# Kernel tuning notes

Hardware: AMD Instinct MI355X
Metric: run time of the kernel (lower is better)

The kernel has to match this reference:

```python
import jax, jax.numpy as jnp
import numpy as np

N_ATOMS = 30000
N_PAIRS = 1200000
N_BASIS = 7
N_RADIAL = 5
N_SPECIES = 119
R_MIN = 0.5
R_MAX = 6.0
UNITS = (512, 512)
BOX = 6.0  # Angstrom box edge so many pairs fall inside the cutoff
N_FEAT = 360  # gaussian-moment feature count for n_radial=5

# static triangular index sets (fully symmetric contractions)
_TRI2_I, _TRI2_J = np.triu_indices(N_RADIAL)
_TRI3 = np.array([(i, j, k) for i in range(N_RADIAL)
                  for j in range(i, N_RADIAL)
                  for k in range(j, N_RADIAL)], dtype=np.int32)


def setup_inputs() -> dict:
    key = jax.random.key(0)
    ks = jax.random.split(key, 8)
    R = jax.random.uniform(ks[0], (N_ATOMS, 3), jnp.float32) * BOX
    Z = jax.random.randint(ks[1], (N_ATOMS,), 0, N_SPECIES, dtype=jnp.int32)
    idx = jax.random.randint(ks[2], (2, N_PAIRS), 0, N_ATOMS, dtype=jnp.int32)
    W_radial = jax.random.normal(ks[3], (N_SPECIES, N_SPECIES, N_RADIAL, N_BASIS), jnp.float32) / np.sqrt(N_BASIS)
    w1 = jax.random.normal(ks[4], (N_FEAT, UNITS[0]), jnp.float32) / np.sqrt(N_FEAT)
    b1 = jnp.zeros((UNITS[0],), jnp.float32)
    w2 = jax.random.normal(ks[5], (UNITS[0], UNITS[1]), jnp.float32) / np.sqrt(UNITS[0])
    b2 = jnp.zeros((UNITS[1],), jnp.float32)
    w3 = jax.random.normal(ks[6], (UNITS[1], 1), jnp.float32) / np.sqrt(UNITS[1])
    b3 = jnp.zeros((1,), jnp.float32)
    scale = 2.0 * jnp.ones((N_SPECIES, 1), jnp.float32)
    shift = 1.0 * jnp.ones((N_SPECIES, 1), jnp.float32)
    return dict(R=R, Z=Z, idx=idx, W_radial=W_radial, w1=w1, b1=b1,
                w2=w2, b2=b2, w3=w3, b3=b3, scale=scale, shift=shift)


def _descriptor(R, Z, idx, W_radial):
    idx_i, idx_j = idx[0], idx[1]
    # pairwise displacement (free-space displacement fn)
    dr_vec = R[idx_j] - R[idx_i]                                  # [P,3]
    dr = jnp.sqrt(jnp.sum(dr_vec * dr_vec, axis=-1) + 1e-12)      # [P]
    dn = dr_vec / (dr + 1e-5)[:, None]                            # unit vectors [P,3]

    # gaussian radial basis
    betta = N_BASIS ** 2 / R_MAX ** 2
    rad_norm = (2.0 * betta / np.pi) ** 0.25
    shifts = R_MIN + (R_MAX - R_MIN) / N_BASIS * jnp.arange(N_BASIS, dtype=jnp.float32)
    basis = rad_norm * jnp.exp(-betta * (dr[:, None] - shifts) ** 2)  # [P,B]

    # cosine cutoff and per species-pair embedding of the basis
    cutoff = 0.5 * (jnp.cos(jnp.pi * dr / R_MAX) + 1.0) * (dr < R_MAX)
    coeffs = W_radial[Z[idx_i], Z[idx_j]]                          # [P,K,B] irregular gather
    radial = jnp.einsum('pkb,pb->pk', coeffs, basis)               # [P,K]
    radial = radial * (cutoff / np.sqrt(N_BASIS))[:, None]

    seg = lambda x: jax.ops.segment_sum(x, idx_i, num_segments=N_ATOMS)
    # geometric moments of order 0..3
    m0 = seg(radial)                                               # [A,K]
    m1 = seg(radial[:, :, None] * dn[:, None, :])                  # [A,K,3]
    dn2 = dn[:, :, None] * dn[:, None, :]                          # [P,3,3]
    m2 = seg(radial[:, :, None, None] * dn2[:, None])              # [A,K,3,3]
    dn3 = dn2[:, :, :, None] * dn[:, None, None, :]                # [P,3,3,3]
    m3 = seg(radial[:, :, None, None, None] * dn3[:, None])        # [A,K,3,3,3]

    # gaussian-moment invariant contractions
    c1 = jnp.einsum('ari,asi->ars', m1, m1)
    c2 = jnp.einsum('arij,asij->ars', m2, m2)
    c3 = jnp.einsum('arijk,asijk->ars', m3, m3)
    c4 = jnp.einsum('arij,asik,atjk->arst', m2, m2, m2)
    c5 = jnp.einsum('ari,asj,atij->arst', m1, m1, m2)
    c6 = jnp.einsum('arijk,asijl,atkl->arst', m3, m3, m2)
    c7 = jnp.einsum('arijk,asij,atk->arst', m3, m2, m1)

    A = m0.shape[0]
    gm = jnp.concatenate([
        m0,
        c1[:, _TRI2_I, _TRI2_J],
        c2[:, _TRI2_I, _TRI2_J],
        c3[:, _TRI2_I, _TRI2_J],
        c4[:, _TRI3[:, 0], _TRI3[:, 1], _TRI3[:, 2]],
        c5[:, _TRI2_I, _TRI2_J, :].reshape(A, -1),
        c6[:, _TRI2_I, _TRI2_J, :].reshape(A, -1),
        c7.reshape(A, -1),
    ], axis=-1)                                                    # [A,360]
    return gm


def reference(R, Z, idx, W_radial, w1, b1, w2, b2, w3, b3, scale, shift):
    gm = _descriptor(R, Z, idx, W_radial)
    h = jax.nn.swish(gm @ w1 + b1)
    h = jax.nn.swish(h @ w2 + b2)
    h = h @ w3 + b3                                                # [A,1]
    return scale[Z] * h + shift[Z]
```

## Files before the change

### kernel.cpp

```cpp
#include <hip/hip_runtime.h>

#define NA      30000
#define MPAD    30080
#define NPAIRS  1200000
#define NB      7
#define NK      5
#define NSP     119
#define NFEAT   360
#define KP1     384
#define NU      512
#define WROWH   40
#define MAXSLOT 120
#define PSTRIDE 128
#define NBK     118
#define BCAP    11520
#define PPB     4688
#define NTILE   235

#define BETTA      1.3611111111111112f
#define RADNORM    0.96481348f
#define SHIFT_STEP 0.7857142857142857f
#define PI_OVER_R  0.5235987755982988f
#define INV_SQRT7  0.3779644730092272f
#define RMAXV      6.0f
#define TCOEF      2.138888888888889f

typedef __attribute__((ext_vector_type(8))) short bf16x8;
typedef __attribute__((ext_vector_type(4))) float f32x4;
typedef __attribute__((ext_vector_type(2))) float f32x2;
typedef __attribute__((ext_vector_type(4))) unsigned int u32x4;
typedef _Float16 h16x2 __attribute__((ext_vector_type(2)));

__device__ __forceinline__ unsigned short f2b(float x) {
    unsigned u = __float_as_uint(x);
    unsigned r = u + 0x7FFF + ((u >> 16) & 1);
    return (unsigned short)(r >> 16);
}

__global__ __launch_bounds__(256)
void k_part(const int* __restrict__ idx, const int* __restrict__ Z,
            int* __restrict__ gcur, int* __restrict__ part) {
    __shared__ int hist[NBK];
    __shared__ int base[NBK];
    int tid = threadIdx.x;
    for (int b = tid; b < NBK; b += 256) hist[b] = 0;
    __syncthreads();
    int p0 = blockIdx.x * PPB;
    int p1 = min(p0 + PPB, NPAIRS);
    for (int p = p0 + tid; p < p1; p += 256)
        atomicAdd(&hist[idx[p] >> 8], 1);
    __syncthreads();
    for (int b = tid; b < NBK; b += 256) {
        base[b] = atomicAdd(&gcur[b], hist[b]);
        hist[b] = 0;
    }
    __syncthreads();
    for (int p = p0 + tid; p < p1; p += 256) {
        int i = idx[p];
        int b = i >> 8;
        int j = idx[NPAIRS + p];
        int zj = Z[j];
        int off = base[b] + atomicAdd(&hist[b], 1);
        if (off < BCAP)
            part[b * BCAP + off] = ((i & 255) << 22) | (zj << 15) | j;
    }
}

__global__ __launch_bounds__(256)
void k_csr(const int* __restrict__ part, const int* __restrict__ gcnt,
           int* __restrict__ counts, int* __restrict__ plist) {
    __shared__ int lp[128 * MAXSLOT];
    __shared__ int lc[128];
    int tid = threadIdx.x;
    int lane = tid & 63, wave = tid >> 6;
    int w = blockIdx.x;
    int cb = w >> 1;
    int par = w & 1;
    for (int t = tid; t < 128; t += 256) lc[t] = 0;
    __syncthreads();
    int n = min(gcnt[cb], BCAP);
    for (int e = tid; e < n; e += 256) {
        int v = part[cb * BCAP + e];
        int iloc = v >> 22;
        if ((iloc >> 7) == par) {
            int i7 = iloc & 127;
            int r = atomicAdd(&lc[i7], 1);
            if (r < MAXSLOT) lp[i7 * MAXSLOT + r] = v & 0x3FFFFF;
        }
    }
    __syncthreads();
    for (int t = tid; t < 128; t += 256) {
        int a = w * 128 + t;
        if (a < NA) counts[a] = min(lc[t], MAXSLOT);
    }
    for (int rr = 0; rr < 32; rr++) {
        int row = wave * 32 + rr;
        int a = w * 128 + row;
        if (a < NA) {
            int n_r = min(lc[row], MAXSLOT);
            for (int c = lane; c < n_r; c += 64)
                plist[(size_t)a * PSTRIDE + c] = lp[row * MAXSLOT + c];
        }
    }
}

#define PREP_W   (NSP*NSP*WROWH)
#define PREP_R   NA
#define PREP_W1  (NU*KP1)
#define PREP_W2  (NU*NU)
#define PREP_TOT (PREP_W + PREP_R + PREP_W1 + PREP_W2)
__global__ void k_prep(const float* __restrict__ W, const float* __restrict__ R,
                       const float* __restrict__ w1, const float* __restrict__ w2,
                       unsigned short* __restrict__ Wp, float* __restrict__ Rp,
                       unsigned short* __restrict__ w1T, unsigned short* __restrict__ w2T,
                       int* __restrict__ gcur, float* __restrict__ out) {
    int i = blockIdx.x * blockDim.x + threadIdx.x;
    if (i < 128) gcur[i] = 0;
    if (i < NA) out[i] = 0.f;
    if (i < PREP_W) {
        int row = i / WROWH, e = i - row * WROWH;
        int k = e >> 3, b = e & 7;
        float v = (b < 7) ? W[row * (NK * NB) + k * NB + b] : 0.f;
        ((_Float16*)Wp)[i] = (_Float16)v;
        return;
    }
    i -= PREP_W;
    if (i < PREP_R) {
        f32x4 v = {R[3*i], R[3*i+1], R[3*i+2], 0.f};
        *(f32x4*)&Rp[4*i] = v;
        return;
    }
    i -= PREP_R;
    if (i < PREP_W1) {
        int c = i / KP1, kp = i - c * KP1;
        w1T[i] = (kp < NFEAT) ? f2b(w1[kp * NU + c]) : (unsigned short)0;
        return;
    }
    i -= PREP_W1;
    if (i < PREP_W2) {
        int c = i >> 9, kp = i & 511;
        w2T[i] = f2b(w2[kp * NU + c]);
    }
}

#define LDM(comp) M[(comp) * 65]

__device__ __forceinline__ void do_c5(const float* M, unsigned short* STrow,
                                      int r, int s, int foff) {
    const int S2[3][3] = {{0,1,2},{1,3,4},{2,4,5}};
    float m1r[3], m1q[3];
#pragma unroll
    for (int i = 0; i < 3; i++) m1r[i] = LDM(r*20+1+i);
#pragma unroll
    for (int i = 0; i < 3; i++) m1q[i] = LDM(s*20+1+i);
    float pre[9];
#pragma unroll
    for (int i = 0; i < 3; i++)
#pragma unroll
        for (int j = 0; j < 3; j++) pre[i*3+j] = m1r[i] * m1q[j];
    for (int t = 0; t < 5; t++) {
        float m2t[6];
#pragma unroll
        for (int u = 0; u < 6; u++) m2t[u] = LDM(t*20+4+u);
        float v = 0.f;
#pragma unroll
        for (int i = 0; i < 3; i++)
#pragma unroll
            for (int j = 0; j < 3; j++)
                v += pre[i*3+j] * m2t[S2[i][j]];
        STrow[foff + t] = f2b(v);
    }
}

__device__ __forceinline__ void do_c6(const float* M, unsigned short* STrow,
                                      int r, int s, int foff) {
    const int S2[3][3] = {{0,1,2},{1,3,4},{2,4,5}};
    const int S3[3][3][3] = {
        {{0,1,2},{1,3,4},{2,4,5}},
        {{1,3,4},{3,6,7},{4,7,8}},
        {{2,4,5},{4,7,8},{5,8,9}}
    };
    float m3r[10];
#pragma unroll
    for (int u = 0; u < 10; u++) m3r[u] = LDM(r*20+10+u);
    float m2q[6];
#pragma unroll
    for (int u = 0; u < 6; u++) m2q[u] = LDM(s*20+4+u);
    float U0 = 0.f, U1 = 0.f, U2 = 0.f;
#pragma unroll
    for (int i = 0; i < 3; i++)
#pragma unroll
        for (int j = 0; j < 3; j++) {
            float ww = m2q[S2[i][j]];
            U0 += m3r[S3[i][j][0]] * ww;
            U1 += m3r[S3[i][j][1]] * ww;
            U2 += m3r[S3[i][j][2]] * ww;
        }
    for (int t = 0; t < 5; t++) {
        float v = U0 * LDM(t*20+1) + U1 * LDM(t*20+2) + U2 * LDM(t*20+3);
        STrow[foff + t] = f2b(v);
    }
}

__device__ __forceinline__ void do_c7(const float* M, unsigned short* STrow,
                                      int r, int s, int foff) {
    const int S2[3][3] = {{0,1,2},{1,3,4},{2,4,5}};
    const int S3[3][3][3] = {
        {{0,1,2},{1,3,4},{2,4,5}},
        {{1,3,4},{3,6,7},{4,7,8}},
        {{2,4,5},{4,7,8},{5,8,9}}
    };
    float m3r[10], m3q[10];
#pragma unroll
    for (int u = 0; u < 10; u++) m3r[u] = LDM(r*20+10+u);
#pragma unroll
    for (int u = 0; u < 10; u++) m3q[u] = LDM(s*20+10+u);
    float T[3][3];
#pragma unroll
    for (int k = 0; k < 3; k++)
#pragma unroll
        for (int l = 0; l < 3; l++) {
            float v = 0.f;
#pragma unroll
            for (int i = 0; i < 3; i++)
#pragma unroll
                for (int j = 0; j < 3; j++)
                    v += m3r[S3[i][j][k]] * m3q[S3[i][j][l]];
            T[k][l] = v;
        }
    for (int t = 0; t < 5; t++) {
        float m2t[6];
#pragma unroll
        for (int u = 0; u < 6; u++) m2t[u] = LDM(t*20+4+u);
        float v = 0.f;
#pragma unroll
        for (int k = 0; k < 3; k++)
#pragma unroll
            for (int l = 0; l < 3; l++)
                v += T[k][l] * m2t[S2[k][l]];
        STrow[foff + t] = f2b(v);
    }
}

__global__ __launch_bounds__(512, 2)
void k_momcon(const float* __restrict__ Rp, const int* __restrict__ Z,
              const unsigned short* __restrict__ WpH, const int* __restrict__ counts,
              const int* __restrict__ plist, unsigned short* __restrict__ gmB) {
    __shared__ float MS[100 * 65];
    __shared__ __align__(4) unsigned short ST[64 * 242];
    int tid = threadIdx.x;
    int g = tid >> 3, q = tid & 7;
    int a0 = blockIdx.x * 64;
    int a = a0 + g;

    if (a < NA) {
        f32x4 ri = *(const f32x4*)&Rp[4*a];
        int Zi = Z[a];
        f32x2 acc[50];
#pragma unroll
        for (int u = 0; u < 50; u++) acc[u] = (f32x2){0.f, 0.f};
        int cnt = min(counts[a], MAXSLOT);
        const int* prow = plist + (size_t)a * PSTRIDE;

        const float DCH[6] = {0.14812156f, 0.027590652f, 0.0051393300f,
                              0.00095730500f, 0.00017831700f, 3.3215300e-05f};

        int pk0 = prow[q & 127];
        int pk1 = prow[(q + 8) & 127];
        int j0c = min(pk0 & 0x7FFF, NA - 1);
        f32x4 rj = *(const f32x4*)&Rp[4 * j0c];

        for (int t = q; t < cnt; t += 8) {
            int pk2 = prow[(t + 16) & 127];
            int j1c = min(pk1 & 0x7FFF, NA - 1);
            f32x4 rjn = *(const f32x4*)&Rp[4 * j1c];

            int Zj = (pk0 >> 15) & 0x7F;
            const u32x4* wv = (const u32x4*)(WpH + (size_t)(Zi * NSP + Zj) * WROWH);
            u32x4 wv0 = wv[0], wv1 = wv[1], wv2 = wv[2], wv3 = wv[3], wv4 = wv[4];
            unsigned wu[20];
#pragma unroll
            for (int c = 0; c < 4; c++) {
                wu[c]      = wv0[c];
                wu[4 + c]  = wv1[c];
                wu[8 + c]  = wv2[c];
                wu[12 + c] = wv3[c];
                wu[16 + c] = wv4[c];
            }

            float dx = rj.x - ri.x, dy = rj.y - ri.y, dz = rj.z - ri.z;
            float d2 = dx*dx + dy*dy + dz*dz + 1e-12f;
            float dr = sqrtf(d2);
            float inv = 1.0f / (dr + 1e-5f);
            float nx = dx*inv, ny = dy*inv, nz = dz*inv;

            float t0 = dr - 0.5f;
            float bb[NB];
            bb[0] = RADNORM * __expf(-BETTA * t0 * t0);
            float Tg = __expf(TCOEF * dr);
#pragma unroll
            for (int b = 0; b < 6; b++) bb[b+1] = bb[b] * Tg * DCH[b];

            float cut = (dr < RMAXV) ? 0.5f * (__cosf(PI_OVER_R * dr) + 1.0f) : 0.0f;
            cut *= INV_SQRT7;

            h16x2 bp[4];
            bp[0] = (h16x2){(_Float16)bb[0], (_Float16)bb[1]};
            bp[1] = (h16x2){(_Float16)bb[2], (_Float16)bb[3]};
            bp[2] = (h16x2){(_Float16)bb[4], (_Float16)bb[5]};
            bp[3] = (h16x2){(_Float16)bb[6], (_Float16)0.0f};

            float rad[NK];
#pragma unroll
            for (int k = 0; k < NK; k++) {
                float s = 0.f;
#if __has_builtin(__builtin_amdgcn_fdot2)
#pragma unroll
                for (int c = 0; c < 4; c++)
                    s = __builtin_amdgcn_fdot2(
                        __builtin_bit_cast(h16x2, wu[k*4 + c]), bp[c], s, false);
#else
#pragma unroll
                for (int c = 0; c < 4; c++) {
                    h16x2 w = __builtin_bit_cast(h16x2, wu[k*4 + c]);
                    s += (float)w.x * (float)bp[c].x + (float)w.y * (float)bp[c].y;
                }
#endif
                rad[k] = s * cut;
            }

            float gg[20];
            gg[0] = 1.f; gg[1] = nx; gg[2] = ny; gg[3] = nz;
            gg[4] = nx*nx; gg[5] = nx*ny; gg[6] = nx*nz; gg[7] = ny*ny; gg[8] = ny*nz; gg[9] = nz*nz;
            gg[10] = gg[4]*nx; gg[11] = gg[4]*ny; gg[12] = gg[4]*nz; gg[13] = gg[5]*ny; gg[14] = gg[5]*nz;
            gg[15] = gg[6]*nz; gg[16] = gg[7]*ny; gg[17] = gg[7]*nz; gg[18] = gg[8]*nz; gg[19] = gg[9]*nz;
            f32x2 g2[10];
#pragma unroll
            for (int u = 0; u < 10; u++) g2[u] = (f32x2){gg[2*u], gg[2*u+1]};
#pragma unroll
            for (int k = 0; k < NK; k++) {
                f32x2 rk = (f32x2){rad[k], rad[k]};
#pragma unroll
                for (int u = 0; u < 10; u++)
                    acc[k*10 + u] += rk * g2[u];
            }
            pk0 = pk1; pk1 = pk2; rj = rjn;
        }
#pragma unroll
        for (int u = 0; u < 50; u++) {
            f32x2 v = acc[u];
            double d = __builtin_bit_cast(double, v);
            d = __shfl_xor(d, 1);
            v += __builtin_bit_cast(f32x2, d);
            d = __builtin_bit_cast(double, v);
            d = __shfl_xor(d, 2);
            v += __builtin_bit_cast(f32x2, d);
            d = __builtin_bit_cast(double, v);
            d = __shfl_xor(d, 4);
            v += __builtin_bit_cast(f32x2, d);
            acc[u] = v;
        }
        if (q == 0) {
#pragma unroll
            for (int u = 0; u < 50; u++) {
                MS[(2*u)     * 65 + g] = acc[u].x;
                MS[(2*u + 1) * 65 + g] = acc[u].y;
            }
        }
    }
    __syncthreads();

    int lane = tid & 63, wave = tid >> 6;
    const float* M = MS + lane;
    unsigned short* STrow = ST + lane * 242;

    if (wave == 0) {
        for (int k = 0; k < 5; k++) STrow[k] = f2b(LDM(k * 20));
        int f = 5;
        for (int r = 0; r < 5; r++)
            for (int s = r; s < 5; s++) {
                float v = 0.f;
#pragma unroll
                for (int i = 0; i < 3; i++) v += LDM(r*20+1+i) * LDM(s*20+1+i);
                STrow[f++] = f2b(v);
            }
        const float W2U[6] = {1,2,2,1,2,1};
        for (int r = 0; r < 5; r++)
            for (int s = r; s < 5; s++) {
                float v = 0.f;
#pragma unroll
                for (int u = 0; u < 6; u++) v += W2U[u] * LDM(r*20+4+u) * LDM(s*20+4+u);
                STrow[f++] = f2b(v);
            }
        const float W3U[10] = {1,3,3,3,6,3,1,3,3,1};
        for (int r = 0; r < 5; r++)
            for (int s = r; s < 5; s++) {
                float v = 0.f;
#pragma unroll
                for (int u = 0; u < 10; u++) v += W3U[u] * LDM(r*20+10+u) * LDM(s*20+10+u);
                STrow[f++] = f2b(v);
            }
        do_c7(M, STrow, 3, 4, 160 + 13*5);
        do_c7(M, STrow, 4, 4, 160 + 14*5);
    } else if (wave == 1 || wave == 2) {
        const int S2[3][3] = {{0,1,2},{1,3,4},{2,4,5}};
        int e0 = (wave == 1) ? 0 : 18, e1 = (wave == 1) ? 18 : 35;
        int e = 0;
        for (int r = 0; r < 5; r++)
            for (int s = r; s < 5; s++)
                for (int t = s; t < 5; t++) {
                    if (e >= e0 && e < e1) {
                        float m2r[6], m2q[6], m2t[6];
#pragma unroll
                        for (int u = 0; u < 6; u++) m2r[u] = LDM(r*20+4+u);
#pragma unroll
                        for (int u = 0; u < 6; u++) m2q[u] = LDM(s*20+4+u);
#pragma unroll
                        for (int u = 0; u < 6; u++) m2t[u] = LDM(t*20+4+u);
                        float v = 0.f;
#pragma unroll
                        for (int i = 0; i < 3; i++)
#pragma unroll
                            for (int j = 0; j < 3; j++)
#pragma unroll
                                for (int k = 0; k < 3; k++)
                                    v += m2r[S2[i][j]] * m2q[S2[i][k]] * m2t[S2[j][k]];
                        STrow[50 + e] = f2b(v);
                    }
                    e++;
                }
    } else if (wave == 3) {
        int p = 0;
        for (int r = 0; r < 5; r++)
            for (int s = r; s < 5; s++) {
                if (p < 8) do_c5(M, STrow, r, s, 85 + p*5);
                p++;
            }
        do_c7(M, STrow, 3, 3, 160 + 12*5);
    } else if (wave == 4) {
        int p = 0;
        for (int r = 0; r < 5; r++)
            for (int s = r; s < 5; s++) {
                if (p >= 8) do_c5(M, STrow, r, s, 85 + p*5);
                p++;
            }
        do_c6(M, STrow, 0, 0, 235);
    } else {
        int pc0 = (wave - 5) * 4;
        int p = 0;
        for (int r = 0; r < 5; r++)
            for (int s = r; s < 5; s++) {
                if (p >= pc0 && p < pc0 + 4) do_c7(M, STrow, r, s, 160 + p*5);
                p++;
            }
    }
    __syncthreads();
    for (int e = tid; e < 64 * 120; e += 512) {
        int row = e / 120, c = e - row * 120;
        if (a0 + row < NA)
            *(unsigned int*)&gmB[(size_t)(a0 + row) * KP1 + 2*c] =
                *(const unsigned int*)&ST[row * 242 + 2*c];
    }
    __syncthreads();

    {
        int g0 = 1 + wave * 3;
        for (int gi = 0; gi < 3; gi++) {
            int gr = g0 + gi;
            int r = gr / 5, s = gr - r * 5;
            do_c6(M, STrow, r, s, 235 + gr*5 - 240);
        }
        if (wave == 0) {
            for (int z = 360; z < 384; z++) STrow[z - 240] = 0;
        }
    }
    __syncthreads();
    for (int e = tid; e < 64 * 72; e += 512) {
        int row = e / 72, c = e - row * 72;
        if (a0 + row < NA)
            *(unsigned int*)&gmB[(size_t)(a0 + row) * KP1 + 240 + 2*c] =
                *(const unsigned int*)&ST[row * 242 + 2*c];
    }
}

__device__ __forceinline__ void stage8(const unsigned short* gp, unsigned short* lp) {
    __builtin_amdgcn_global_load_lds(
        (const __attribute__((address_space(1))) unsigned int*)gp,
        (__attribute__((address_space(3))) unsigned int*)lp, 16, 0, 0);
}

template<int KPAD, int MODE>
__global__ __launch_bounds__(512) void k_mfma(const unsigned short* __restrict__ A,
                                              const unsigned short* __restrict__ B,
                                              const float* __restrict__ bias,
                                              const float* __restrict__ w3,
                                              void* __restrict__ outp) {
    __shared__ __align__(16) unsigned char SMEM[35072];
    unsigned short* As = (unsigned short*)SMEM;
    unsigned short* Bs = (unsigned short*)(SMEM + 16384);
    float* red = (float*)(SMEM + 32768);
    int tid = threadIdx.x;
    int lane = tid & 63, wave = tid >> 6;
    int wm = wave >> 1, wn = wave & 1;
    int quad = lane >> 4, l16 = lane & 15;
    int lrow = lane >> 3;
    int lchk = lane & 7;

    int bid = blockIdx.x;
    int xcd = bid & 7, rr_ = bid >> 3;
    int cblk = rr_ & 3, agrp = rr_ >> 2;
    int atile = xcd * 30 + agrp;
    if (atile >= NTILE) return;

    int rowA0, rowB0;
    if (MODE == 1) { rowA0 = atile * 128; rowB0 = cblk * 128; }
    else           { rowA0 = cblk * 128;  rowB0 = atile * 128; }

    f32x4 acc[2][4];
    f32x4 zero = {0.f, 0.f, 0.f, 0.f};
#pragma unroll
    for (int i = 0; i < 2; i++)
#pragma unroll
        for (int j = 0; j < 4; j++) acc[i][j] = zero;

    for (int k0 = 0; k0 < KPAD; k0 += 64) {
        __syncthreads();
#pragma unroll
        for (int i = 0; i < 2; i++) {
            int r = wave * 16 + i * 8 + lrow;
            int gc = lchk ^ (r & 7);
            stage8(A + (size_t)(rowA0 + r) * KPAD + k0 + gc * 8, &As[(wave * 16 + i * 8) * 64]);
        }
#pragma unroll
        for (int i = 0; i < 2; i++) {
            int r = wave * 16 + i * 8 + lrow;
            int gc = lchk ^ (r & 7);
            stage8(B + (size_t)(rowB0 + r) * KPAD + k0 + gc * 8, &Bs[(wave * 16 + i * 8) * 64]);
        }
        __syncthreads();
#pragma unroll
        for (int s = 0; s < 2; s++) {
            bf16x8 af[2], bfr[4];
#pragma unroll
            for (int mt = 0; mt < 2; mt++) {
                int r = wm * 32 + mt * 16 + l16;
                af[mt] = *(const bf16x8*)&As[r * 64 + (((s * 4 + quad) ^ (r & 7)) * 8)];
            }
#pragma unroll
            for (int nt = 0; nt < 4; nt++) {
                int r = wn * 64 + nt * 16 + l16;
                bfr[nt] = *(const bf16x8*)&Bs[r * 64 + (((s * 4 + quad) ^ (r & 7)) * 8)];
            }
#pragma unroll
            for (int mt = 0; mt < 2; mt++)
#pragma unroll
                for (int nt = 0; nt < 4; nt++)
                    acc[mt][nt] = __builtin_amdgcn_mfma_f32_16x16x32_bf16(
                        af[mt], bfr[nt], acc[mt][nt], 0, 0, 0);
        }
    }

    if (MODE == 1) {
        __syncthreads();
        unsigned short* Ot = (unsigned short*)SMEM;
#pragma unroll
        for (int nt = 0; nt < 4; nt++) {
            int c_loc = wn * 64 + nt * 16 + l16;
            float b = bias[rowB0 + c_loc];
#pragma unroll
            for (int mt = 0; mt < 2; mt++) {
#pragma unroll
                for (int reg = 0; reg < 4; reg++) {
                    int a_loc = wm * 32 + mt * 16 + quad * 4 + reg;
                    float v = acc[mt][nt][reg] + b;
                    Ot[a_loc * 136 + c_loc] = f2b(v / (1.f + __expf(-v)));
                }
            }
        }
        __syncthreads();
        unsigned short* O = (unsigned short*)outp;
        int half = lane >> 5, l32 = lane & 31;
#pragma unroll
        for (int it = 0; it < 8; it++) {
            int rloc = wave * 16 + it * 2 + half;
            int a = rowA0 + rloc;
            unsigned long long d = *(const unsigned long long*)&Ot[rloc * 136 + l32 * 4];
            if (a < NA)
                *(unsigned long long*)&O[(size_t)a * NU + rowB0 + l32 * 4] = d;
        }
    } else {
        float pn[4] = {0.f, 0.f, 0.f, 0.f};
#pragma unroll
        for (int mt = 0; mt < 2; mt++) {
#pragma unroll
            for (int reg = 0; reg < 4; reg++) {
                int c = rowA0 + wm * 32 + mt * 16 + quad * 4 + reg;
                float b = bias[c];
                float w3c = w3[c];
#pragma unroll
                for (int nt = 0; nt < 4; nt++) {
                    float v = acc[mt][nt][reg] + b;
                    pn[nt] += w3c * (v / (1.f + __expf(-v)));
                }
            }
        }
#pragma unroll
        for (int nt = 0; nt < 4; nt++) {
            pn[nt] += __shfl_xor(pn[nt], 16);
            pn[nt] += __shfl_xor(pn[nt], 32);
        }
        __syncthreads();
        if (quad == 0) {
#pragma unroll
            for (int nt = 0; nt < 4; nt++)
                red[(wave * 4 + nt) * 16 + l16] = pn[nt];
        }
        __syncthreads();
        if (tid < 128) {
            int wn2 = tid >> 6, nt2 = (tid >> 4) & 3, lb = tid & 15;
            float s = 0.f;
#pragma unroll
            for (int w4 = 0; w4 < 4; w4++)
                s += red[((w4 * 2 + wn2) * 4 + nt2) * 16 + lb];
            int a = rowB0 + wn2 * 64 + nt2 * 16 + lb;
            if (a < NA) atomicAdd((float*)outp + a, s);
        }
    }
}

__global__ void k_finish(float* __restrict__ out, const float* __restrict__ b3,
                         const int* __restrict__ Z, const float* __restrict__ scale,
                         const float* __restrict__ shift) {
    int a = blockIdx.x * blockDim.x + threadIdx.x;
    if (a >= NA) return;
    int z = Z[a];
    out[a] = scale[z] * (out[a] + b3[0]) + shift[z];
}

extern "C" void kernel_launch(void* const* d_in, const int* in_sizes, int n_in,
                              void* d_out, int out_size, void* d_ws, size_t ws_size,
                              hipStream_t stream) {
    const float* R    = (const float*)d_in[0];
    const int*   Z    = (const int*)  d_in[1];
    const int*   idx  = (const int*)  d_in[2];
    const float* Wr   = (const float*)d_in[3];
    const float* w1   = (const float*)d_in[4];
    const float* b1   = (const float*)d_in[5];
    const float* w2   = (const float*)d_in[6];
    const float* b2   = (const float*)d_in[7];
    const float* w3   = (const float*)d_in[8];
    const float* b3   = (const float*)d_in[9];
    const float* scale= (const float*)d_in[10];
    const float* shift= (const float*)d_in[11];
    float* out = (float*)d_out;
    char* ws = (char*)d_ws;

    int*            gcur   = (int*)  (ws + 0);
    int*            counts = (int*)  (ws + 512);
    int*            part   = (int*)  (ws + 120576);
    int*            plist  = (int*)  (ws + 5558016);
    unsigned short* gmB    = (unsigned short*)(ws + 32918016);
    unsigned short* w1T    = (unsigned short*)(ws + 56019456);
    unsigned short* w2T    = (unsigned short*)(ws + 56412672);
    unsigned short* h1B    = (unsigned short*)(ws + 56936960);
    unsigned short* WpH    = (unsigned short*)(ws + 87738880);
    float*          Rpad   = (float*)(ws + 89778064);

    k_prep   <<<(PREP_TOT + 255) / 256, 256, 0, stream>>>(Wr, R, w1, w2, WpH, Rpad,
                                                          w1T, w2T, gcur, out);
    k_part   <<<256, 256, 0, stream>>>(idx, Z, gcur, part);
    k_csr    <<<235, 256, 0, stream>>>(part, gcur, counts, plist);
    k_momcon <<<(NA + 63) / 64, 512, 0, stream>>>(Rpad, Z, WpH, counts, plist, gmB);

    k_mfma<KP1, 1><<<960, 512, 0, stream>>>(gmB, w1T, b1, nullptr, (void*)h1B);
    k_mfma<NU,  2><<<960, 512, 0, stream>>>(w2T, h1B, b2, w3, (void*)out);

    k_finish<<<(NA + 255) / 256, 256, 0, stream>>>(out, b3, Z, scale, shift);
}
```

Before: 246.3 us.

## Double-buffer MFMA GEMM LDS tiles with K-step of 32 and prefetch

Restructures the MLP GEMM main loop to use two LDS buffers, each holding a K-slice of 32, and prefetches the next slice with global_load_lds while MFMAs run on the current one. This leaves one barrier per iteration instead of two, and it uses a new 4-chunk XOR swizzle. The goal is to hide global load latency behind compute. In exchange, each iteration does half as much MFMA work, and the prefetch is issued asynchronously without waiting on vmcnt before the barrier, which could be a correctness risk.

```diff
diff --git a/kernel.cpp b/kernel.cpp
--- a/kernel.cpp
+++ b/kernel.cpp
@@ -496,15 +496,13 @@
                                               const float* __restrict__ w3,
                                               void* __restrict__ outp) {
     __shared__ __align__(16) unsigned char SMEM[35072];
-    unsigned short* As = (unsigned short*)SMEM;
-    unsigned short* Bs = (unsigned short*)(SMEM + 16384);
+    unsigned short* AsB = (unsigned short*)SMEM;
+    unsigned short* BsB = (unsigned short*)(SMEM + 16384);
     float* red = (float*)(SMEM + 32768);
     int tid = threadIdx.x;
     int lane = tid & 63, wave = tid >> 6;
     int wm = wave >> 1, wn = wave & 1;
     int quad = lane >> 4, l16 = lane & 15;
-    int lrow = lane >> 3;
-    int lchk = lane & 7;
 
     int bid = blockIdx.x;
     int xcd = bid & 7, rr_ = bid >> 3;
@@ -516,6 +514,13 @@
     if (MODE == 1) { rowA0 = atile * 128; rowB0 = cblk * 128; }
     else           { rowA0 = cblk * 128;  rowB0 = atile * 128; }
 
+    int srow = wave * 16 + (lane >> 2);
+    int sch  = lane & 3;
+    int skey = (srow & 3) ^ ((srow >> 2) & 3);
+    int sgc  = sch ^ skey;
+    const unsigned short* gA = A + (size_t)(rowA0 + srow) * KPAD + sgc * 8;
+    const unsigned short* gB = B + (size_t)(rowB0 + srow) * KPAD + sgc * 8;
+
     f32x4 acc[2][4];
     f32x4 zero = {0.f, 0.f, 0.f, 0.f};
 #pragma unroll
@@ -523,45 +528,44 @@
 #pragma unroll
         for (int j = 0; j < 4; j++) acc[i][j] = zero;
 
-    for (int k0 = 0; k0 < KPAD; k0 += 64) {
+    stage8(gA, AsB + wave * 512);
+    stage8(gB, BsB + wave * 512);
+    __syncthreads();
+
+    const int NT = KPAD / 32;
+    int keyR = (l16 & 3) ^ ((l16 >> 2) & 3);
+    int cur = 0;
+    for (int t = 0; t < NT; t++) {
+        if (t + 1 < NT) {
+            int nb = cur ^ 1;
+            stage8(gA + (t + 1) * 32, AsB + nb * 4096 + wave * 512);
+            stage8(gB + (t + 1) * 32, BsB + nb * 4096 + wave * 512);
+        }
+        const unsigned short* Ac = AsB + cur * 4096;
+        const unsigned short* Bc = BsB + cur * 4096;
+        int slot = (quad ^ keyR) & 3;
+        bf16x8 af[2], bfr[4];
+#pragma unroll
+        for (int mt = 0; mt < 2; mt++) {
+            int r = wm * 32 + mt * 16 + l16;
+            af[mt] = *(const bf16x8*)&Ac[r * 32 + slot * 8];
+        }
+#pragma unroll
+        for (int nt = 0; nt < 4; nt++) {
+            int r = wn * 64 + nt * 16 + l16;
+            bfr[nt] = *(const bf16x8*)&Bc[r * 32 + slot * 8];
+        }
+#pragma unroll
+        for (int mt = 0; mt < 2; mt++)
+#pragma unroll
+            for (int nt = 0; nt < 4; nt++)
+                acc[mt][nt] = __builtin_amdgcn_mfma_f32_16x16x32_bf16(
+                    af[mt], bfr[nt], acc[mt][nt], 0, 0, 0);
         __syncthreads();
-#pragma unroll
-        for (int i = 0; i < 2; i++) {
-            int r = wave * 16 + i * 8 + lrow;
-            int gc = lchk ^ (r & 7);
-            stage8(A + (size_t)(rowA0 + r) * KPAD + k0 + gc * 8, &As[(wave * 16 + i * 8) * 64]);
-        }
-#pragma unroll
-        for (int i = 0; i < 2; i++) {
-            int r = wave * 16 + i * 8 + lrow;
-            int gc = lchk ^ (r & 7);
-            stage8(B + (size_t)(rowB0 + r) * KPAD + k0 + gc * 8, &Bs[(wave * 16 + i * 8) * 64]);
-        }
-        __syncthreads();
-#pragma unroll
-        for (int s = 0; s < 2; s++) {
-            bf16x8 af[2], bfr[4];
-#pragma unroll
-            for (int mt = 0; mt < 2; mt++) {
-                int r = wm * 32 + mt * 16 + l16;
-                af[mt] = *(const bf16x8*)&As[r * 64 + (((s * 4 + quad) ^ (r & 7)) * 8)];
-            }
-#pragma unroll
-            for (int nt = 0; nt < 4; nt++) {
-                int r = wn * 64 + nt * 16 + l16;
-                bfr[nt] = *(const bf16x8*)&Bs[r * 64 + (((s * 4 + quad) ^ (r & 7)) * 8)];
-            }
-#pragma unroll
-            for (int mt = 0; mt < 2; mt++)
-#pragma unroll
-                for (int nt = 0; nt < 4; nt++)
-                    acc[mt][nt] = __builtin_amdgcn_mfma_f32_16x16x32_bf16(
-                        af[mt], bfr[nt], acc[mt][nt], 0, 0, 0);
-        }
+        cur ^= 1;
     }
 
     if (MODE == 1) {
-        __syncthreads();
         unsigned short* Ot = (unsigned short*)SMEM;
 #pragma unroll
         for (int nt = 0; nt < 4; nt++) {
@@ -609,7 +613,6 @@
             pn[nt] += __shfl_xor(pn[nt], 16);
             pn[nt] += __shfl_xor(pn[nt], 32);
         }
-        __syncthreads();
         if (quad == 0) {
 #pragma unroll
             for (int nt = 0; nt < 4; nt++)
```

Result: no change. 247.8 us (+0.6%).
